# Performance work log

Hardware: AMD Instinct MI355X
Metric: run time of the kernel (lower is better)

The kernel has to match this reference:

```python
import jax, jax.numpy as jnp
import numpy as np

B, S, D, H = 4, 1024, 1024, 16
HS = D // H  # head_size = 64


def setup_inputs() -> dict:
    key = jax.random.key(0)
    ks = jax.random.split(key, 12)
    sc_d = 1.0 / np.sqrt(D)
    sc_h = 1.0 / np.sqrt(HS)
    inp = {
        "queries": jax.random.normal(ks[0], (B, S, D), jnp.float32),
        "keys": jax.random.normal(ks[1], (B, S, D), jnp.float32),
        "values": jax.random.normal(ks[2], (B, S, D), jnp.float32),
        # causal mask: scores where mask == 0 are filled with -1e9
        "mask": jnp.tril(jnp.ones((S, S), jnp.int32)),
        # per-head query/key projections: [H, D, HS] weights, [H, HS] biases
        "Wq": jax.random.uniform(ks[3], (H, D, HS), jnp.float32, -sc_d, sc_d),
        "bq": jax.random.uniform(ks[4], (H, HS), jnp.float32, -sc_d, sc_d),
        "Wk": jax.random.uniform(ks[5], (H, D, HS), jnp.float32, -sc_d, sc_d),
        "bk": jax.random.uniform(ks[6], (H, HS), jnp.float32, -sc_d, sc_d),
        # shared value projection: [D, HS]
        "Wv": jax.random.uniform(ks[7], (D, HS), jnp.float32, -sc_d, sc_d),
        "bv": jax.random.uniform(ks[8], (HS,), jnp.float32, -sc_d, sc_d),
        # output projection: [HS, D]
        "Wo": jax.random.uniform(ks[9], (HS, D), jnp.float32, -sc_h, sc_h),
        "bo": jax.random.uniform(ks[10], (D,), jnp.float32, -sc_h, sc_h),
    }
    return inp


def reference(queries, keys, values, mask, Wq, bq, Wk, bk, Wv, bv, Wo, bo):
    # shared value projection: [B, S, HS]
    v = jnp.einsum("bsd,de->bse", values, Wv) + bv
    # batched per-head projections (replaces the python loop over heads)
    q = jnp.einsum("bsd,hde->bhse", queries, Wq) + bq[None, :, None, :]
    k = jnp.einsum("btd,hde->bhte", keys, Wk) + bk[None, :, None, :]
    scores = jnp.einsum("bhse,bhte->bhst", q, k) / jnp.sqrt(jnp.float32(HS))
    scores = jnp.where(mask == 0, jnp.float32(-1e9), scores)
    attn = jax.nn.softmax(scores, axis=-1)  # [B, H, S, S]; dropout = eval-mode identity
    head_out = jnp.einsum("bhst,bte->bhse", attn, v)
    out = head_out.mean(axis=1)  # mean over heads -> [B, S, HS]
    out = jnp.einsum("bse,ed->bsd", out, Wo) + bo
    attention_weights = attn.mean(axis=1)  # [B, S, S]
    return out, attention_weights
```

## Files before the change

### kernel.cpp

```cpp
#include <hip/hip_runtime.h>
#include <hip/hip_bf16.h>
#include <stdint.h>

typedef _Float16 half8 __attribute__((ext_vector_type(8)));
typedef _Float16 half4 __attribute__((ext_vector_type(4)));
typedef float    f32x4 __attribute__((ext_vector_type(4)));

#define MFMA16(a, b, c) __builtin_amdgcn_mfma_f32_16x16x32_f16(a, b, c, 0, 0, 0)

typedef __attribute__((address_space(1))) const void GVOID;
typedef __attribute__((address_space(3))) void LVOID;
__device__ __forceinline__ void glds16(const void* g, void* l)
{
    __builtin_amdgcn_global_load_lds((GVOID*)g, (LVOID*)l, 16, 0, 0);
}

#define BARRIER() do { asm volatile("" ::: "memory"); \
    __builtin_amdgcn_s_barrier(); \
    asm volatile("" ::: "memory"); } while (0)

__global__ __launch_bounds__(256) void prep_all(
    const float* __restrict__ Wq, const float* __restrict__ Wk,
    const float* __restrict__ Wv, const float* __restrict__ Wo,
    const float* __restrict__ queries, const float* __restrict__ keys,
    _Float16* __restrict__ WqkT, _Float16* __restrict__ WvT,
    _Float16* __restrict__ WoT, _Float16* __restrict__ a16,
    float* __restrict__ vbuf, float* __restrict__ ctx,
    float* __restrict__ attn)
{
    __shared__ float t[32][33];
    const int id = blockIdx.x;
    const int tid = threadIdx.x;

    if (id < 2176) {
        const float* X; _Float16* Y; int R, C, bx, by;
        if (id < 2048) {
            const int isK = id >> 10;
            const int local = id & 1023;
            bx = local & 1;
            by = (local >> 1) & 31;
            const int hz = local >> 6;
            X = (isK ? Wk : Wq) + (long)hz * 65536;
            Y = WqkT + (long)isK * 1048576 + (long)hz * 65536;
            R = 1024; C = 64;
        } else if (id < 2112) {
            const int local = id - 2048;
            bx = local & 1; by = local >> 1;
            X = Wv; Y = WvT; R = 1024; C = 64;
        } else {
            const int local = id - 2112;
            bx = local & 31; by = local >> 5;
            X = Wo; Y = WoT; R = 64; C = 1024;
        }
        const int c0 = bx * 32, r0 = by * 32;
        const int tx = tid & 31, ty = tid >> 5;
#pragma unroll
        for (int i = 0; i < 4; ++i)
            t[ty + i * 8][tx] = X[(long)(r0 + ty + i * 8) * C + c0 + tx];
        __syncthreads();
#pragma unroll
        for (int i = 0; i < 4; ++i)
            Y[(long)(c0 + ty + i * 8) * R + r0 + tx] = (_Float16)t[tx][ty + i * 8];
    } else if (id < 6272) {
        const int isK = (id - 2176) >> 11;
        const int local = (id - 2176) & 2047;
        const float* S = isK ? keys : queries;
        _Float16* Dz = a16 + (long)isK * 4194304;
        const long i = ((long)local * 256 + tid) * 8;
        const float4 v0 = *(const float4*)(S + i);
        const float4 v1 = *(const float4*)(S + i + 4);
        half8 h;
        h[0] = (_Float16)v0.x; h[1] = (_Float16)v0.y;
        h[2] = (_Float16)v0.z; h[3] = (_Float16)v0.w;
        h[4] = (_Float16)v1.x; h[5] = (_Float16)v1.y;
        h[6] = (_Float16)v1.z; h[7] = (_Float16)v1.w;
        *(half8*)(Dz + i) = h;
    } else if (id < 6528) {
        const float4 z = {0.f, 0.f, 0.f, 0.f};
        ((float4*)vbuf)[(long)(id - 6272) * 256 + tid] = z;
    } else if (id < 6784) {
        const float4 z = {0.f, 0.f, 0.f, 0.f};
        ((float4*)ctx)[(long)(id - 6528) * 256 + tid] = z;
    } else {
        const float4 z = {0.f, 0.f, 0.f, 0.f};
        ((float4*)attn)[(long)(id - 6784) * 256 + tid] = z;
    }
}

__global__ __launch_bounds__(256) void transpose_to_f16(
    const float* __restrict__ X, _Float16* __restrict__ Y,
    int R, int C, long inBS, long outBS)
{
    __shared__ float t[32][33];
    const int bz = blockIdx.z;
    X += (long)bz * inBS;
    Y += (long)bz * outBS;
    const int c0 = blockIdx.x * 32, r0 = blockIdx.y * 32;
    const int tx = threadIdx.x & 31, ty = threadIdx.x >> 5;
#pragma unroll
    for (int i = 0; i < 4; ++i)
        t[ty + i * 8][tx] = X[(long)(r0 + ty + i * 8) * C + c0 + tx];
    __syncthreads();
#pragma unroll
    for (int i = 0; i < 4; ++i)
        Y[(long)(c0 + ty + i * 8) * R + r0 + tx] = (_Float16)t[tx][ty + i * 8];
}

__global__ __launch_bounds__(256, 2) void gemm_qk_glds(
    const _Float16* __restrict__ A16,
    const _Float16* __restrict__ BT,
    const float* __restrict__ bias0, const float* __restrict__ bias1,
    _Float16* __restrict__ Cout)
{
    __shared__ __align__(16) _Float16 As[2][128 * 64];
    __shared__ __align__(16) _Float16 Bs[2][128 * 64];

    const int gx  = gridDim.x, gy = gridDim.y;
    const int nwg = gx * gy * (int)gridDim.z;
    const int lid = (int)blockIdx.x + gx * ((int)blockIdx.y + gy * (int)blockIdx.z);
    const int q8  = nwg >> 3;
    const int xcd = lid & 7, loc = lid >> 3;
    const int sw  = xcd * q8 + loc;
    const int nt  = sw % gx;
    const int tm2 = sw / gx;
    const int mt  = tm2 % gy;
    const int z   = tm2 / gy;

    const int n0 = nt * 128;
    const int m0 = mt * 128;
    const int tid  = threadIdx.x;
    const int wave = tid >> 6, lane = tid & 63;
    const int m16  = lane & 15, quad = lane >> 4;

    const char* Az = (const char*)(A16 + (long)z * 4194304);
    const char* Bz = (const char*)(BT  + (long)z * 1048576);

    const int colbyte = (((lane & 7) ^ (lane >> 3)) << 4);
    const char* gaBase = Az + ((long)(m0 + wave * 32 + (lane >> 3)) << 11) + colbyte;
    const char* gbBase = Bz + ((long)(n0 + wave * 32 + (lane >> 3)) << 11) + colbyte;

    f32x4 acc[2][8];
    {
        f32x4 zz = {0.f, 0.f, 0.f, 0.f};
#pragma unroll
        for (int i = 0; i < 2; ++i)
#pragma unroll
            for (int j = 0; j < 8; ++j) acc[i][j] = zz;
    }

    auto STAGE = [&](int bf, int k0) {
        const char* ga = gaBase + (k0 << 1);
        const char* gb = gbBase + (k0 << 1);
        _Float16* la = &As[bf][wave * 32 * 64];
        _Float16* lb = &Bs[bf][wave * 32 * 64];
#pragma unroll
        for (int i = 0; i < 4; ++i) {
            glds16(ga + (long)i * 8 * 2048, la + i * 8 * 64);
            glds16(gb + (long)i * 8 * 2048, lb + i * 8 * 64);
        }
    };

    auto COMPUTE = [&](int bf) {
        const char* Ab = (const char*)&As[bf][0];
        const char* Bp = (const char*)&Bs[bf][0];
        const int sw4 = (m16 & 7) << 4;
#pragma unroll
        for (int kss = 0; kss < 2; ++kss) {
            const int kbs = (kss * 64 + quad * 16) ^ sw4;
            const half8 a0 = *(const half8*)(Ab + (wave * 32 + m16) * 128 + kbs);
            const half8 a1 = *(const half8*)(Ab + (wave * 32 + 16 + m16) * 128 + kbs);
#pragma unroll
            for (int c = 0; c < 8; ++c) {
                const half8 bfr = *(const half8*)(Bp + (c * 16 + m16) * 128 + kbs);
                acc[0][c] = MFMA16(a0, bfr, acc[0][c]);
                acc[1][c] = MFMA16(a1, bfr, acc[1][c]);
            }
        }
    };

    STAGE(0, 0);
    STAGE(1, 64);
    int cur = 0;
    for (int t = 0; t < 15; ++t) {
        asm volatile("s_waitcnt vmcnt(8)" ::: "memory");
        __builtin_amdgcn_sched_barrier(0);
        BARRIER();
        COMPUTE(cur);
        BARRIER();
        if (t < 14) STAGE(cur, (t + 2) * 64);
        cur ^= 1;
    }
    asm volatile("s_waitcnt vmcnt(0)" ::: "memory");
    __builtin_amdgcn_sched_barrier(0);
    BARRIER();
    COMPUTE(cur);

    const float* bias = z ? bias1 : bias0;
    _Float16* Cz = Cout + (long)z * 4194304;
#pragma unroll
    for (int hh = 0; hh < 2; ++hh) {
#pragma unroll
        for (int c = 0; c < 8; ++c) {
            const int col = n0 + c * 16 + m16;
            const float bb = bias[col];
#pragma unroll
            for (int r = 0; r < 4; ++r) {
                const int row = m0 + wave * 32 + hh * 16 + quad * 4 + r;
                Cz[(long)row * 1024 + col] = (_Float16)(acc[hh][c][r] + bb);
            }
        }
    }
}

__global__ __launch_bounds__(256, 2) void gemm_f16_v2(
    const float* __restrict__ A0, const float* __restrict__ A1,
    const _Float16* __restrict__ BT,
    const float* __restrict__ bias0, const float* __restrict__ bias1,
    void* __restrict__ Cout,
    int N, int lda, int ldbt, int ldc,
    long aBS, long bBS, long cBS,
    int c_half, int atomic, int nks, int kchunk)
{
    __shared__ __align__(16) _Float16 As[128][72];
    __shared__ __align__(16) _Float16 Bs[128][72];

    const int gx  = gridDim.x, gy = gridDim.y;
    const int nwg = gx * gy * (int)gridDim.z;
    const int lid = (int)blockIdx.x + gx * ((int)blockIdx.y + gy * (int)blockIdx.z);
    const int q8  = nwg >> 3, r8 = nwg & 7;
    const int xcd = lid & 7, loc = lid >> 3;
    const int sw  = (xcd < r8 ? xcd * (q8 + 1) : r8 * (q8 + 1) + (xcd - r8) * q8) + loc;
    const int nt  = sw % gx;
    const int tm2 = sw / gx;
    const int mt  = tm2 % gy;
    const int bz  = tm2 / gy;

    const int b = bz / nks, ks = bz % nks;
    const int kbeg = ks * kchunk;
    const int kend = kbeg + kchunk;

    const float* A = A1 ? (b ? A1 : A0) : (A0 + (long)b * aBS);
    const _Float16* Bb = BT + (long)b * bBS;

    const int n0 = nt * 128;
    const int m0 = mt * 128;
    const int tid  = threadIdx.x;
    const int wave = tid >> 6, lane = tid & 63;
    const int m16  = lane & 15, quad = lane >> 4;

    const int acol = (tid & 15) * 4;
    const int arb  = tid >> 4;
    const int bj   = tid >> 1;
    const int bcc  = (tid & 1) * 32;
    int jn = n0 + bj; if (jn > N - 1) jn = N - 1;
    const _Float16* bpB = Bb + (long)jn * ldbt;

    f32x4 acc[2][8];
    {
        f32x4 zz = {0.f, 0.f, 0.f, 0.f};
#pragma unroll
        for (int i = 0; i < 2; ++i)
#pragma unroll
            for (int j = 0; j < 8; ++j) acc[i][j] = zz;
    }

    for (int k0 = kbeg; k0 < kend; k0 += 64) {
        {
            float4 av[8];
#pragma unroll
            for (int p = 0; p < 8; ++p)
                av[p] = *(const float4*)(A + (long)(m0 + arb + p * 16) * lda + k0 + acol);
#pragma unroll
            for (int p = 0; p < 8; ++p) {
                half4 hv;
                hv[0] = (_Float16)av[p].x; hv[1] = (_Float16)av[p].y;
                hv[2] = (_Float16)av[p].z; hv[3] = (_Float16)av[p].w;
                *(half4*)&As[arb + p * 16][acol] = hv;
            }
        }
        {
            const _Float16* bp = bpB + k0 + bcc;
            half8 b0 = *(const half8*)(bp);
            half8 b1 = *(const half8*)(bp + 8);
            half8 b2 = *(const half8*)(bp + 16);
            half8 b3 = *(const half8*)(bp + 24);
            *(half8*)&Bs[bj][bcc]      = b0;
            *(half8*)&Bs[bj][bcc + 8]  = b1;
            *(half8*)&Bs[bj][bcc + 16] = b2;
            *(half8*)&Bs[bj][bcc + 24] = b3;
        }
        __syncthreads();
#pragma unroll
        for (int kss = 0; kss < 2; ++kss) {
            const int ko = kss * 32 + quad * 8;
            const half8 a0 = *(const half8*)&As[wave * 32 + m16][ko];
            const half8 a1 = *(const half8*)&As[wave * 32 + 16 + m16][ko];
#pragma unroll
            for (int c = 0; c < 8; ++c) {
                const half8 bf = *(const half8*)&Bs[c * 16 + m16][ko];
                acc[0][c] = MFMA16(a0, bf, acc[0][c]);
                acc[1][c] = MFMA16(a1, bf, acc[1][c]);
            }
        }
        __syncthreads();
    }

    const float* bias = b ? bias1 : bias0;
    const int addb = (bias != nullptr) && (kbeg == 0);
#pragma unroll
    for (int hh = 0; hh < 2; ++hh) {
#pragma unroll
        for (int c = 0; c < 8; ++c) {
            const int col = n0 + c * 16 + m16;
            if (col >= N) continue;
            const float bb = addb ? bias[col] : 0.f;
#pragma unroll
            for (int r = 0; r < 4; ++r) {
                const int row = m0 + wave * 32 + hh * 16 + quad * 4 + r;
                const float v = acc[hh][c][r] + bb;
                const long idx = (long)b * cBS + (long)row * ldc + col;
                if (atomic)      atomicAdd(&((float*)Cout)[idx], v);
                else if (c_half) ((_Float16*)Cout)[idx] = (_Float16)v;
                else             ((float*)Cout)[idx] = v;
            }
        }
    }
}

__global__ __launch_bounds__(256, 4) void attn_stats(
    const _Float16* __restrict__ q_all, const _Float16* __restrict__ k_all,
    float* __restrict__ m_out, float* __restrict__ il_out)
{
    const int st = blockIdx.x, h = blockIdx.y, b = blockIdx.z;
    const int tid = threadIdx.x, wave = tid >> 6, lane = tid & 63;
    const int m16 = lane & 15, quad = lane >> 4;
    const int s0 = st * 64;
    const int sw = s0 + wave * 16;

    __shared__ __align__(16) _Float16 qs[64][72];
    __shared__ __align__(16) _Float16 ks[128][72];

    const int srow = tid >> 2;
    const int scol = (tid & 3) * 16;

    {
        const _Float16* qsrc = q_all + ((long)(b * 1024 + s0 + srow)) * 1024 + h * 64 + scol;
        *(half8*)&qs[srow][scol]     = *(const half8*)(qsrc);
        *(half8*)&qs[srow][scol + 8] = *(const half8*)(qsrc + 8);
    }

    const _Float16* ksrcb = k_all + ((long)(b * 1024 + srow)) * 1024 + h * 64 + scol;

    float mr[4], lr[4];
#pragma unroll
    for (int r = 0; r < 4; ++r) { mr[r] = -3.0e38f; lr[r] = 0.f; }

    half8 a0, a1;
    for (int ch = 0; 2 * ch <= st; ++ch) {
        const int tbase = 2 * ch;
        const int two = (tbase + 1 <= st);

        const _Float16* ksrc0 = ksrcb + (long)(tbase * 64) * 1024;
        const half8 k0 = *(const half8*)(ksrc0);
        const half8 k1 = *(const half8*)(ksrc0 + 8);
        half8 k2, k3;
        if (two) {
            const _Float16* ksrc1 = ksrc0 + (long)64 * 1024;
            k2 = *(const half8*)(ksrc1);
            k3 = *(const half8*)(ksrc1 + 8);
        }

        __syncthreads();
        *(half8*)&ks[srow][scol]     = k0;
        *(half8*)&ks[srow][scol + 8] = k1;
        if (two) {
            *(half8*)&ks[64 + srow][scol]     = k2;
            *(half8*)&ks[64 + srow][scol + 8] = k3;
        }
        __syncthreads();

        if (ch == 0) {
            a0 = *(const half8*)&qs[wave * 16 + m16][quad * 8];
            a1 = *(const half8*)&qs[wave * 16 + m16][quad * 8 + 32];
        }

        const int ncol = two ? 8 : 4;
        for (int c = 0; c < ncol; ++c) {
            const half8 b0 = *(const half8*)&ks[c * 16 + m16][quad * 8];
            const half8 b1 = *(const half8*)&ks[c * 16 + m16][quad * 8 + 32];
            f32x4 cc = {0.f, 0.f, 0.f, 0.f};
            cc = MFMA16(a0, b0, cc);
            cc = MFMA16(a1, b1, cc);
            const int tile = tbase + (c >> 2);
            if (tile < st) {
#pragma unroll
                for (int r = 0; r < 4; ++r) {
                    const float zz = cc[r] * 0.125f;
                    const float nm = fmaxf(mr[r], zz);
                    lr[r] = lr[r] * __expf(mr[r] - nm) + __expf(zz - nm);
                    mr[r] = nm;
                }
            } else {
                const int col = tile * 64 + (c & 3) * 16 + m16;
#pragma unroll
                for (int r = 0; r < 4; ++r) {
                    const int row = sw + quad * 4 + r;
                    if (col <= row) {
                        const float zz = cc[r] * 0.125f;
                        const float nm = fmaxf(mr[r], zz);
                        lr[r] = lr[r] * __expf(mr[r] - nm) + __expf(zz - nm);
                        mr[r] = nm;
                    }
                }
            }
        }
    }

#pragma unroll
    for (int mk = 1; mk < 16; mk <<= 1) {
#pragma unroll
        for (int r = 0; r < 4; ++r) {
            const float om = __shfl_xor(mr[r], mk);
            const float ol = __shfl_xor(lr[r], mk);
            const float nm = fmaxf(mr[r], om);
            lr[r] = lr[r] * __expf(mr[r] - nm) + ol * __expf(om - nm);
            mr[r] = nm;
        }
    }
    if (m16 == 0) {
#pragma unroll
        for (int r = 0; r < 4; ++r) {
            const long idx = ((long)(b * 16 + h)) * 1024 + sw + quad * 4 + r;
            m_out[idx]  = mr[r];
            il_out[idx] = 1.f / lr[r];
        }
    }
}

__global__ __launch_bounds__(256, 3) void attn_pmean(
    const _Float16* __restrict__ q_all, const _Float16* __restrict__ k_all,
    const float* __restrict__ m_in, const float* __restrict__ il_in,
    const _Float16* __restrict__ vT,
    float* __restrict__ attn,
    float* __restrict__ ctx)
{
    const int ttile = blockIdx.x, stile = blockIdx.y, b = blockIdx.z;
    const int tid = threadIdx.x;
    if (ttile > stile) return;

    __shared__ __align__(16) _Float16 qs2[2][64 * 64];
    __shared__ __align__(16) _Float16 ks2[2][64 * 64];
    __shared__ __align__(16) _Float16 ps[64][72];
    __shared__ __align__(16) float mls[16][64];
    __shared__ __align__(16) float ils[16][64];

    const int wave = tid >> 6, lane = tid & 63;
    const int m16 = lane & 15, quad = lane >> 4;
    const int s0 = stile * 64;
    const int t0 = ttile * 64;
    const int sw = s0 + wave * 16;
    const int diag = (ttile == stile);

    {
        const int hh = tid >> 4;
        const int c4 = (tid & 15) * 4;
        const long ix = ((long)(b * 16 + hh)) * 1024 + s0 + c4;
        const float4 mv4 = *(const float4*)&m_in[ix];
        const float4 iv4 = *(const float4*)&il_in[ix];
        *(float4*)&mls[hh][c4] = mv4;
        *(float4*)&ils[hh][c4] = iv4;
    }

    const int colb = (((lane & 7) ^ (lane >> 3)) << 4);
    const char* gq = (const char*)q_all + ((long)(b * 1024 + s0 + wave * 16 + (lane >> 3)) << 11) + colb;
    const char* gk = (const char*)k_all + ((long)(b * 1024 + t0 + wave * 16 + (lane >> 3)) << 11) + colb;

    auto STAGE_P = [&](int bf, int h) {
        const char* q = gq + h * 128;
        const char* k = gk + h * 128;
        _Float16* lq = &qs2[bf][wave * 16 * 64];
        _Float16* lk = &ks2[bf][wave * 16 * 64];
        glds16(q, lq);
        glds16(q + 8 * 2048, lq + 8 * 64);
        glds16(k, lk);
        glds16(k + 8 * 2048, lk + 8 * 64);
    };

    STAGE_P(0, 0);
    STAGE_P(1, 1);
    asm volatile("s_waitcnt lgkmcnt(0)" ::: "memory");
    BARRIER();

    float pm[4][4];
#pragma unroll
    for (int c = 0; c < 4; ++c)
#pragma unroll
        for (int r = 0; r < 4; ++r) pm[c][r] = 0.f;

    const int swz = (m16 & 7) << 4;
    int cur = 0;

    auto COMPUTE_H = [&](int h, int bf) {
        const char* Qc = (const char*)&qs2[bf][0];
        const char* Kc = (const char*)&ks2[bf][0];
        const half8 a0 = *(const half8*)(Qc + (wave * 16 + m16) * 128 + ((quad * 16) ^ swz));
        const half8 a1 = *(const half8*)(Qc + (wave * 16 + m16) * 128 + ((quad * 16 + 64) ^ swz));
        const float4 mv = *(const float4*)&mls[h][wave * 16 + quad * 4];
        const float4 iv = *(const float4*)&ils[h][wave * 16 + quad * 4];
        const float mrow[4] = {mv.x, mv.y, mv.z, mv.w};
        const float irow[4] = {iv.x, iv.y, iv.z, iv.w};
        if (!diag) {
#pragma unroll
            for (int c = 0; c < 4; ++c) {
                const half8 b0 = *(const half8*)(Kc + (c * 16 + m16) * 128 + ((quad * 16) ^ swz));
                const half8 b1 = *(const half8*)(Kc + (c * 16 + m16) * 128 + ((quad * 16 + 64) ^ swz));
                f32x4 cc = {0.f, 0.f, 0.f, 0.f};
                cc = MFMA16(a0, b0, cc);
                cc = MFMA16(a1, b1, cc);
#pragma unroll
                for (int r = 0; r < 4; ++r)
                    pm[c][r] += __expf(cc[r] * 0.125f - mrow[r]) * irow[r];
            }
        } else {
#pragma unroll
            for (int c = 0; c < 4; ++c) {
                const half8 b0 = *(const half8*)(Kc + (c * 16 + m16) * 128 + ((quad * 16) ^ swz));
                const half8 b1 = *(const half8*)(Kc + (c * 16 + m16) * 128 + ((quad * 16 + 64) ^ swz));
                f32x4 cc = {0.f, 0.f, 0.f, 0.f};
                cc = MFMA16(a0, b0, cc);
                cc = MFMA16(a1, b1, cc);
                const int col = t0 + c * 16 + m16;
#pragma unroll
                for (int r = 0; r < 4; ++r) {
                    const int row = sw + quad * 4 + r;
                    if (col <= row)
                        pm[c][r] += __expf(cc[r] * 0.125f - mrow[r]) * irow[r];
                }
            }
        }
    };

    for (int h = 0; h < 15; ++h) {
        asm volatile("s_waitcnt vmcnt(4)" ::: "memory");
        __builtin_amdgcn_sched_barrier(0);
        BARRIER();
        COMPUTE_H(h, cur);
        BARRIER();
        if (h < 14) STAGE_P(cur, h + 2);
        cur ^= 1;
    }
    asm volatile("s_waitcnt vmcnt(0)" ::: "memory");
    __builtin_amdgcn_sched_barrier(0);
    BARRIER();
    COMPUTE_H(15, cur);

#pragma unroll
    for (int c = 0; c < 4; ++c) {
#pragma unroll
        for (int r = 0; r < 4; ++r) {
            const int rloc = (wave << 4) + (quad << 2) + r;
            const int cloc = c * 16 + m16;
            const float p = pm[c][r] * 0.0625f;
            attn[((long)(b * 1024 + s0 + rloc)) * 1024 + t0 + cloc] = p;
            ps[rloc][cloc] = (_Float16)p;
        }
    }
    __syncthreads();

    const _Float16* vTb = vT + (long)b * 65536 + t0;
    f32x4 apv[4];
    {
        f32x4 zz = {0.f, 0.f, 0.f, 0.f};
#pragma unroll
        for (int c = 0; c < 4; ++c) apv[c] = zz;
    }
#pragma unroll
    for (int kss = 0; kss < 2; ++kss) {
        const half8 a = *(const half8*)&ps[wave * 16 + m16][kss * 32 + quad * 8];
#pragma unroll
        for (int c = 0; c < 4; ++c) {
            const half8 bf = *(const half8*)(vTb + (long)(c * 16 + m16) * 1024 + kss * 32 + quad * 8);
            apv[c] = MFMA16(a, bf, apv[c]);
        }
    }
#pragma unroll
    for (int c = 0; c < 4; ++c) {
#pragma unroll
        for (int r = 0; r < 4; ++r) {
            const int row = sw + quad * 4 + r;
            const int e   = c * 16 + m16;
            atomicAdd(&ctx[((long)(b * 1024 + row)) * 64 + e], apv[c][r]);
        }
    }
}

extern "C" void kernel_launch(void* const* d_in, const int* in_sizes, int n_in,
                              void* d_out, int out_size, void* d_ws, size_t ws_size,
                              hipStream_t stream)
{
    const float* queries = (const float*)d_in[0];
    const float* keys    = (const float*)d_in[1];
    const float* values  = (const float*)d_in[2];
    const float* Wq = (const float*)d_in[4];
    const float* bq = (const float*)d_in[5];
    const float* Wk = (const float*)d_in[6];
    const float* bk = (const float*)d_in[7];
    const float* Wv = (const float*)d_in[8];
    const float* bv = (const float*)d_in[9];
    const float* Wo = (const float*)d_in[10];
    const float* bo = (const float*)d_in[11];

    float* out_ptr  = (float*)d_out;
    float* attn_ptr = out_ptr + (long)4096 * 1024;

    uint8_t* w = (uint8_t*)d_ws;
    size_t off = 0;
    auto alloc = [&](size_t bytes) {
        void* p = w + off;
        off = (off + bytes + 255) & ~(size_t)255;
        return p;
    };
    _Float16* WqkT  = (_Float16*)alloc((size_t)2 * 1024 * 1024 * 2);
    _Float16* WvT   = (_Float16*)alloc((size_t)64 * 1024 * 2);
    _Float16* WoT   = (_Float16*)alloc((size_t)1024 * 64 * 2);
    _Float16* qkall = (_Float16*)alloc((size_t)2 * 4194304 * 2);
    _Float16* a16   = (_Float16*)alloc((size_t)2 * 4194304 * 2);
    float*    vbuf  = (float*)alloc((size_t)4096 * 64 * 4);
    _Float16* vT    = (_Float16*)alloc((size_t)4 * 64 * 1024 * 2);
    float*    ctx   = (float*)alloc((size_t)4096 * 64 * 4);
    float*    mbuf  = (float*)alloc((size_t)65536 * 4);
    float*    ilbuf = (float*)alloc((size_t)65536 * 4);
    (void)ws_size; (void)in_sizes; (void)n_in; (void)out_size;

    _Float16* qall = qkall;
    _Float16* kall = qkall + (long)4194304;

    prep_all<<<dim3(10880, 1, 1), 256, 0, stream>>>(
        Wq, Wk, Wv, Wo, queries, keys,
        WqkT, WvT, WoT, a16, vbuf, ctx, attn_ptr);

    gemm_qk_glds<<<dim3(8, 32, 2), 256, 0, stream>>>(
        a16, WqkT, bq, bk, qkall);

    gemm_f16_v2<<<dim3(1, 32, 8), 256, 0, stream>>>(
        values, nullptr, WvT, bv, nullptr, vbuf,
        64, 1024, 1024, 64,
        0, 0, 0,
        0, 1, 8, 128);

    transpose_to_f16<<<dim3(2, 32, 4), 256, 0, stream>>>(vbuf, vT, 1024, 64, 65536, 65536);

    attn_stats<<<dim3(16, 16, 4), 256, 0, stream>>>(qall, kall, mbuf, ilbuf);
    attn_pmean<<<dim3(16, 16, 4), 256, 0, stream>>>(qall, kall, mbuf, ilbuf, vT, attn_ptr, ctx);

    gemm_f16_v2<<<dim3(8, 32, 1), 256, 0, stream>>>(
        ctx, nullptr, WoT, bo, nullptr, out_ptr,
        1024, 64, 64, 1024,
        0, 0, 0,
        0, 0, 1, 64);
}
```

Before: 235.5 us.

## Fuse V projection and transpose into QK projection kernel; reuse LDS in pmean

Merges the value projection GEMM and the transpose-to-f16 step into the QK projection launch. The first 32 blocks compute V directly, writing transposed f16 output and skipping the fp32 vbuf round trip and its zeroing. This removes two kernel launches and intermediate memory traffic. In attn_pmean the probability tile now reuses the qs2 LDS buffer with an XOR swizzle, and launch bounds rise to 4 waves per SIMD for occupancy. The V blocks use a simple unpipelined loop and could become stragglers.

Result: faster. 229.8 us (-2.4%).

```diff
diff --git a/kernel.cpp b/kernel.cpp
--- a/kernel.cpp
+++ b/kernel.cpp
@@ -25,8 +25,7 @@
     const float* __restrict__ queries, const float* __restrict__ keys,
     _Float16* __restrict__ WqkT, _Float16* __restrict__ WvT,
     _Float16* __restrict__ WoT, _Float16* __restrict__ a16,
-    float* __restrict__ vbuf, float* __restrict__ ctx,
-    float* __restrict__ attn)
+    float* __restrict__ ctx, float* __restrict__ attn)
 {
     __shared__ float t[32][33];
     const int id = blockIdx.x;
@@ -77,60 +76,120 @@
         *(half8*)(Dz + i) = h;
     } else if (id < 6528) {
         const float4 z = {0.f, 0.f, 0.f, 0.f};
-        ((float4*)vbuf)[(long)(id - 6272) * 256 + tid] = z;
-    } else if (id < 6784) {
-        const float4 z = {0.f, 0.f, 0.f, 0.f};
-        ((float4*)ctx)[(long)(id - 6528) * 256 + tid] = z;
+        ((float4*)ctx)[(long)(id - 6272) * 256 + tid] = z;
     } else {
         const float4 z = {0.f, 0.f, 0.f, 0.f};
-        ((float4*)attn)[(long)(id - 6784) * 256 + tid] = z;
+        ((float4*)attn)[(long)(id - 6528) * 256 + tid] = z;
     }
 }
 
-__global__ __launch_bounds__(256) void transpose_to_f16(
-    const float* __restrict__ X, _Float16* __restrict__ Y,
-    int R, int C, long inBS, long outBS)
-{
-    __shared__ float t[32][33];
-    const int bz = blockIdx.z;
-    X += (long)bz * inBS;
-    Y += (long)bz * outBS;
-    const int c0 = blockIdx.x * 32, r0 = blockIdx.y * 32;
-    const int tx = threadIdx.x & 31, ty = threadIdx.x >> 5;
-#pragma unroll
-    for (int i = 0; i < 4; ++i)
-        t[ty + i * 8][tx] = X[(long)(r0 + ty + i * 8) * C + c0 + tx];
-    __syncthreads();
-#pragma unroll
-    for (int i = 0; i < 4; ++i)
-        Y[(long)(c0 + ty + i * 8) * R + r0 + tx] = (_Float16)t[tx][ty + i * 8];
-}
-
-__global__ __launch_bounds__(256, 2) void gemm_qk_glds(
+__global__ __launch_bounds__(256, 2) void qk_vproj(
     const _Float16* __restrict__ A16,
     const _Float16* __restrict__ BT,
     const float* __restrict__ bias0, const float* __restrict__ bias1,
-    _Float16* __restrict__ Cout)
+    _Float16* __restrict__ Cout,
+    const float* __restrict__ values,
+    const _Float16* __restrict__ WvT,
+    const float* __restrict__ bv,
+    _Float16* __restrict__ vT)
 {
-    __shared__ __align__(16) _Float16 As[2][128 * 64];
-    __shared__ __align__(16) _Float16 Bs[2][128 * 64];
-
-    const int gx  = gridDim.x, gy = gridDim.y;
-    const int nwg = gx * gy * (int)gridDim.z;
-    const int lid = (int)blockIdx.x + gx * ((int)blockIdx.y + gy * (int)blockIdx.z);
-    const int q8  = nwg >> 3;
-    const int xcd = lid & 7, loc = lid >> 3;
-    const int sw  = xcd * q8 + loc;
-    const int nt  = sw % gx;
-    const int tm2 = sw / gx;
-    const int mt  = tm2 % gy;
-    const int z   = tm2 / gy;
+    __shared__ __align__(16) char smem[65536];
+    const int lid = blockIdx.x;
+    const int tid = threadIdx.x;
+    const int wave = tid >> 6, lane = tid & 63;
+    const int m16  = lane & 15, quad = lane >> 4;
+
+    if (lid < 32) {
+        _Float16 (*As)[72] = (_Float16(*)[72])smem;
+        _Float16 (*Bs)[72] = (_Float16(*)[72])(smem + 128 * 72 * 2);
+        const int mt = lid;
+        const int m0 = mt * 128;
+
+        const int acol = (tid & 15) * 4;
+        const int arb  = tid >> 4;
+        const int bj   = tid >> 1;
+        const int bcc  = (tid & 1) * 32;
+        const int jn = (bj > 63) ? 63 : bj;
+        const _Float16* bpB = WvT + (long)jn * 1024;
+
+        f32x4 acc[2][8];
+        {
+            f32x4 zz = {0.f, 0.f, 0.f, 0.f};
+#pragma unroll
+            for (int i = 0; i < 2; ++i)
+#pragma unroll
+                for (int j = 0; j < 8; ++j) acc[i][j] = zz;
+        }
+
+        for (int k0 = 0; k0 < 1024; k0 += 64) {
+            {
+                float4 av[8];
+#pragma unroll
+                for (int p = 0; p < 8; ++p)
+                    av[p] = *(const float4*)(values + (long)(m0 + arb + p * 16) * 1024 + k0 + acol);
+#pragma unroll
+                for (int p = 0; p < 8; ++p) {
+                    half4 hv;
+                    hv[0] = (_Float16)av[p].x; hv[1] = (_Float16)av[p].y;
+                    hv[2] = (_Float16)av[p].z; hv[3] = (_Float16)av[p].w;
+                    *(half4*)&As[arb + p * 16][acol] = hv;
+                }
+            }
+            {
+                const _Float16* bp = bpB + k0 + bcc;
+                half8 b0 = *(const half8*)(bp);
+                half8 b1 = *(const half8*)(bp + 8);
+                half8 b2 = *(const half8*)(bp + 16);
+                half8 b3 = *(const half8*)(bp + 24);
+                *(half8*)&Bs[bj][bcc]      = b0;
+                *(half8*)&Bs[bj][bcc + 8]  = b1;
+                *(half8*)&Bs[bj][bcc + 16] = b2;
+                *(half8*)&Bs[bj][bcc + 24] = b3;
+            }
+            __syncthreads();
+#pragma unroll
+            for (int kss = 0; kss < 2; ++kss) {
+                const int ko = kss * 32 + quad * 8;
+                const half8 a0 = *(const half8*)&As[wave * 32 + m16][ko];
+                const half8 a1 = *(const half8*)&As[wave * 32 + 16 + m16][ko];
+#pragma unroll
+                for (int c = 0; c < 4; ++c) {
+                    const half8 bf = *(const half8*)&Bs[c * 16 + m16][ko];
+                    acc[0][c] = MFMA16(a0, bf, acc[0][c]);
+                    acc[1][c] = MFMA16(a1, bf, acc[1][c]);
+                }
+            }
+            __syncthreads();
+        }
+
+#pragma unroll
+        for (int hh = 0; hh < 2; ++hh) {
+#pragma unroll
+            for (int c = 0; c < 4; ++c) {
+                const int e  = c * 16 + m16;
+                const float bb = bv[e];
+#pragma unroll
+                for (int r = 0; r < 4; ++r) {
+                    const int row = m0 + wave * 32 + hh * 16 + quad * 4 + r;
+                    const int b = row >> 10, tt = row & 1023;
+                    vT[(long)b * 65536 + (long)e * 1024 + tt] =
+                        (_Float16)(acc[hh][c][r] + bb);
+                }
+            }
+        }
+        return;
+    }
+
+    const int lid2 = lid - 32;
+    const int xcd = lid2 & 7, loc = lid2 >> 3;
+    const int sw  = xcd * 64 + loc;
+    const int nt  = sw & 7;
+    const int tm2 = sw >> 3;
+    const int mt  = tm2 & 31;
+    const int z   = tm2 >> 5;
 
     const int n0 = nt * 128;
     const int m0 = mt * 128;
-    const int tid  = threadIdx.x;
-    const int wave = tid >> 6, lane = tid & 63;
-    const int m16  = lane & 15, quad = lane >> 4;
 
     const char* Az = (const char*)(A16 + (long)z * 4194304);
     const char* Bz = (const char*)(BT  + (long)z * 1048576);
@@ -151,8 +210,8 @@
     auto STAGE = [&](int bf, int k0) {
         const char* ga = gaBase + (k0 << 1);
         const char* gb = gbBase + (k0 << 1);
-        _Float16* la = &As[bf][wave * 32 * 64];
-        _Float16* lb = &Bs[bf][wave * 32 * 64];
+        _Float16* la = (_Float16*)(smem + bf * 16384) + wave * 32 * 64;
+        _Float16* lb = (_Float16*)(smem + 32768 + bf * 16384) + wave * 32 * 64;
 #pragma unroll
         for (int i = 0; i < 4; ++i) {
             glds16(ga + (long)i * 8 * 2048, la + i * 8 * 64);
@@ -161,8 +220,8 @@
     };
 
     auto COMPUTE = [&](int bf) {
-        const char* Ab = (const char*)&As[bf][0];
-        const char* Bp = (const char*)&Bs[bf][0];
+        const char* Ab = smem + bf * 16384;
+        const char* Bp = smem + 32768 + bf * 16384;
         const int sw4 = (m16 & 7) << 4;
 #pragma unroll
         for (int kss = 0; kss < 2; ++kss) {
@@ -437,7 +496,7 @@
     }
 }
 
-__global__ __launch_bounds__(256, 3) void attn_pmean(
+__global__ __launch_bounds__(256, 4) void attn_pmean(
     const _Float16* __restrict__ q_all, const _Float16* __restrict__ k_all,
     const float* __restrict__ m_in, const float* __restrict__ il_in,
     const _Float16* __restrict__ vT,
@@ -450,7 +509,6 @@
 
     __shared__ __align__(16) _Float16 qs2[2][64 * 64];
     __shared__ __align__(16) _Float16 ks2[2][64 * 64];
-    __shared__ __align__(16) _Float16 ps[64][72];
     __shared__ __align__(16) float mls[16][64];
     __shared__ __align__(16) float ils[16][64];
 
@@ -553,21 +611,29 @@
     __builtin_amdgcn_sched_barrier(0);
     BARRIER();
     COMPUTE_H(15, cur);
-
-#pragma unroll
-    for (int c = 0; c < 4; ++c) {
-#pragma unroll
-        for (int r = 0; r < 4; ++r) {
-            const int rloc = (wave << 4) + (quad << 2) + r;
-            const int cloc = c * 16 + m16;
-            const float p = pm[c][r] * 0.0625f;
-            attn[((long)(b * 1024 + s0 + rloc)) * 1024 + t0 + cloc] = p;
-            ps[rloc][cloc] = (_Float16)p;
-        }
-    }
     __syncthreads();
 
+    {
+        char* Pb = (char*)&qs2[0][0];
+#pragma unroll
+        for (int c = 0; c < 4; ++c) {
+#pragma unroll
+            for (int r = 0; r < 4; ++r) {
+                const int rloc = (wave << 4) + (quad << 2) + r;
+                const int cloc = c * 16 + m16;
+                const float p = pm[c][r] * 0.0625f;
+                attn[((long)(b * 1024 + s0 + rloc)) * 1024 + t0 + cloc] = p;
+                const int chunk = (cloc >> 3) ^ (rloc & 7);
+                *(_Float16*)(Pb + rloc * 128 + (chunk << 4) + (cloc & 7) * 2) =
+                    (_Float16)p;
+            }
+        }
+    }
+    __syncthreads();
+
     const _Float16* vTb = vT + (long)b * 65536 + t0;
+    const char* Pb = (const char*)&qs2[0][0];
+    const int Rr = wave * 16 + m16;
     f32x4 apv[4];
     {
         f32x4 zz = {0.f, 0.f, 0.f, 0.f};
@@ -576,7 +642,8 @@
     }
 #pragma unroll
     for (int kss = 0; kss < 2; ++kss) {
-        const half8 a = *(const half8*)&ps[wave * 16 + m16][kss * 32 + quad * 8];
+        const int chunk = (kss * 4 + quad) ^ (Rr & 7);
+        const half8 a = *(const half8*)(Pb + Rr * 128 + (chunk << 4));
 #pragma unroll
         for (int c = 0; c < 4; ++c) {
             const half8 bf = *(const half8*)(vTb + (long)(c * 16 + m16) * 1024 + kss * 32 + quad * 8);
@@ -625,7 +692,6 @@
     _Float16* WoT   = (_Float16*)alloc((size_t)1024 * 64 * 2);
     _Float16* qkall = (_Float16*)alloc((size_t)2 * 4194304 * 2);
     _Float16* a16   = (_Float16*)alloc((size_t)2 * 4194304 * 2);
-    float*    vbuf  = (float*)alloc((size_t)4096 * 64 * 4);
     _Float16* vT    = (_Float16*)alloc((size_t)4 * 64 * 1024 * 2);
     float*    ctx   = (float*)alloc((size_t)4096 * 64 * 4);
     float*    mbuf  = (float*)alloc((size_t)65536 * 4);
@@ -635,22 +701,15 @@
     _Float16* qall = qkall;
     _Float16* kall = qkall + (long)4194304;
 
-    prep_all<<<dim3(10880, 1, 1), 256, 0, stream>>>(
+    prep_all<<<dim3(10624, 1, 1), 256, 0, stream>>>(
         Wq, Wk, Wv, Wo, queries, keys,
-        WqkT, WvT, WoT, a16, vbuf, ctx, attn_ptr);
-
-    gemm_qk_glds<<<dim3(8, 32, 2), 256, 0, stream>>>(
-        a16, WqkT, bq, bk, qkall);
-
-    gemm_f16_v2<<<dim3(1, 32, 8), 256, 0, stream>>>(
-        values, nullptr, WvT, bv, nullptr, vbuf,
-        64, 1024, 1024, 64,
-        0, 0, 0,
-        0, 1, 8, 128);
-
-    transpose_to_f16<<<dim3(2, 32, 4), 256, 0, stream>>>(vbuf, vT, 1024, 64, 65536, 65536);
+        WqkT, WvT, WoT, a16, ctx, attn_ptr);
+
+    qk_vproj<<<dim3(544, 1, 1), 256, 0, stream>>>(
+        a16, WqkT, bq, bk, qkall, values, WvT, bv, vT);
 
     attn_stats<<<dim3(16, 16, 4), 256, 0, stream>>>(qall, kall, mbuf, ilbuf);
+
     attn_pmean<<<dim3(16, 16, 4), 256, 0, stream>>>(qall, kall, mbuf, ilbuf, vT, attn_ptr, ctx);
 
     gemm_f16_v2<<<dim3(8, 32, 1), 256, 0, stream>>>(
```
